# Performance work log

Measured on AMD Instinct MI355X. Metric: run time of the kernel, lower is better.

The kernel has to match this reference:

```python
import jax, jax.numpy as jnp
import numpy as np

RNN_HID = 64
INPUT_DIM = 35
SEQ_LEN = 48
BATCH = 4096


def setup_inputs() -> dict:
    key = jax.random.key(0)
    ks = jax.random.split(key, 16)
    x_t = jax.random.normal(ks[0], (BATCH, SEQ_LEN, INPUT_DIM), jnp.float32)
    masks = (jax.random.uniform(ks[1], (BATCH, SEQ_LEN, INPUT_DIM)) > 0.2).astype(jnp.float32)
    deltas = jax.random.uniform(ks[2], (BATCH, SEQ_LEN, INPUT_DIM), jnp.float32)
    evals = jax.random.normal(ks[3], (BATCH, SEQ_LEN, INPUT_DIM), jnp.float32)
    eval_masks = (jax.random.uniform(ks[4], (BATCH, SEQ_LEN, INPUT_DIM)) > 0.8).astype(jnp.float32)
    is_train = jnp.ones((BATCH,), jnp.float32)

    in_sz = INPUT_DIM * 2  # LSTMCell input = concat(x_c, m)
    s_lstm = 1.0 / np.sqrt(RNN_HID)
    # torch LSTMCell params: W_ih [4H, in], W_hh [4H, H], b_ih [4H], b_hh [4H]
    W_ih = jax.random.uniform(ks[5], (4 * RNN_HID, in_sz), jnp.float32, -s_lstm, s_lstm)
    W_hh = jax.random.uniform(ks[6], (4 * RNN_HID, RNN_HID), jnp.float32, -s_lstm, s_lstm)
    b_ih = jax.random.uniform(ks[7], (4 * RNN_HID,), jnp.float32, -s_lstm, s_lstm)
    b_hh = jax.random.uniform(ks[8], (4 * RNN_HID,), jnp.float32, -s_lstm, s_lstm)
    W_reg = jax.random.uniform(ks[9], (INPUT_DIM, RNN_HID), jnp.float32, -s_lstm, s_lstm)
    b_reg = jax.random.uniform(ks[10], (INPUT_DIM,), jnp.float32, -s_lstm, s_lstm)
    # TemporalDecay: W [RNN_HID, input_dim], b [RNN_HID]
    W_td = jax.random.uniform(ks[11], (RNN_HID, INPUT_DIM), jnp.float32, -s_lstm, s_lstm)
    b_td = jax.random.uniform(ks[12], (RNN_HID,), jnp.float32, -s_lstm, s_lstm)
    # out Linear(RNN_HID -> 1)
    W_out = jax.random.uniform(ks[13], (1, RNN_HID), jnp.float32, -s_lstm, s_lstm)
    b_out = jax.random.uniform(ks[14], (1,), jnp.float32, -s_lstm, s_lstm)
    return {
        'x_t': x_t, 'masks': masks, 'deltas': deltas, 'evals': evals,
        'eval_masks': eval_masks, 'is_train': is_train,
        'W_ih': W_ih, 'W_hh': W_hh, 'b_ih': b_ih, 'b_hh': b_hh,
        'W_reg': W_reg, 'b_reg': b_reg, 'W_td': W_td, 'b_td': b_td,
        'W_out': W_out, 'b_out': b_out,
    }


def _lstm_cell(inp, h, c, W_ih, W_hh, b_ih, b_hh):
    # gates ordered i, f, g, o as in torch.nn.LSTMCell
    gates = inp @ W_ih.T + h @ W_hh.T + b_ih + b_hh  # [B, 4H]
    i, f, g, o = jnp.split(gates, 4, axis=-1)
    i = jax.nn.sigmoid(i)
    f = jax.nn.sigmoid(f)
    g = jnp.tanh(g)
    o = jax.nn.sigmoid(o)
    c_new = f * c + i * g
    h_new = o * jnp.tanh(c_new)
    return h_new, c_new


def reference(x_t, masks, deltas, evals, eval_masks, is_train,
              W_ih, W_hh, b_ih, b_hh, W_reg, b_reg, W_td, b_td, W_out, b_out):
    B, T, D = x_t.shape
    h0 = jnp.zeros((B, RNN_HID), x_t.dtype)
    c0 = jnp.zeros((B, RNN_HID), x_t.dtype)

    def step(carry, xs):
        h, c, x_loss = carry
        x, m, d = xs  # each [B, D]
        x_hat = h @ W_reg.T + b_reg
        x_c = m * x + (1.0 - m) * x_hat
        x_loss = x_loss + jnp.sum(jnp.abs(x - x_hat) * m) / (jnp.sum(m) + 1e-5)
        inputs = jnp.concatenate([x_c, m], axis=1)  # [B, 2D]
        # temporal decay (computed as in original, result unused)
        gamma = jnp.exp(-jax.nn.relu(d @ W_td.T + b_td))
        h, c = _lstm_cell(inputs, h, c, W_ih, W_hh, b_ih, b_hh)
        return (h, c, x_loss), x_c

    xs = (jnp.swapaxes(x_t, 0, 1), jnp.swapaxes(masks, 0, 1), jnp.swapaxes(deltas, 0, 1))
    (h, c, x_loss), imp = jax.lax.scan(step, (h0, c0, jnp.float32(0.0)), xs)
    imputations = jnp.swapaxes(imp, 0, 1)  # [B, T, D]
    y_h = jax.nn.sigmoid(h @ W_out.T + b_out)
    loss = x_loss / T  # y_loss == 0
    return loss, y_h, imputations
```

## Files before the change

kernel.cpp:

```cpp
#include <hip/hip_runtime.h>
#include <stdint.h>

#define B_    4096
#define T_    48
#define D_    35
#define KROW  168
#define ROWEL (T_ * D_)
#define L2E   1.44269504f

typedef float f32x4 __attribute__((ext_vector_type(4)));
typedef short bf16x8 __attribute__((ext_vector_type(8)));

static __device__ __forceinline__ uint32_t fbits(float x){union{float f;uint32_t u;}v;v.f=x;return v.u;}
static __device__ __forceinline__ float bitsf(uint32_t u){union{uint32_t u;float f;}v;v.u=u;return v.f;}
static __device__ __forceinline__ float bf2f(unsigned short b){return bitsf(((uint32_t)b)<<16);}
static __device__ __forceinline__ unsigned short f2bf_rne(float x){
    uint32_t u=fbits(x); return (unsigned short)((u+0x7fffu+((u>>16)&1u))>>16);
}
static __device__ __forceinline__ float rcp_(float x){return __builtin_amdgcn_rcpf(x);}
static __device__ __forceinline__ float exp2_(float x){return __builtin_amdgcn_exp2f(x);}

#define MFMA __builtin_amdgcn_mfma_f32_16x16x32_bf16


__global__ __launch_bounds__(512, 1)
void brits_main(const float* __restrict__ x_t, const float* __restrict__ masks,
                const float* __restrict__ W_ih, const float* __restrict__ W_hh,
                const float* __restrict__ b_ih, const float* __restrict__ b_hh,
                const float* __restrict__ W_reg, const float* __restrict__ b_reg,
                const float* __restrict__ W_out, const float* __restrict__ b_out,
                float* __restrict__ ws, float* __restrict__ out)
{
    __shared__ __align__(16) unsigned short Abuf[2][16 * KROW];
    __shared__ __align__(16) unsigned short stash[16 * ROWEL];
    __shared__ unsigned long long mbits[16 * T_];
    __shared__ float lsum[T_ * 3 * 64];
    __shared__ float wout[65];

    const int tid    = threadIdx.x;
    const int lane   = tid & 63;
    const int w      = tid >> 6;
    const int g      = lane >> 4;
    const int cc     = lane & 15;
    const int batch0 = blockIdx.x * 16;
    const int u      = (w & 3) * 16 + cc;
    const int u2     = (w - 4) * 16 + cc;

    for (int i = tid; i < 16 * KROW; i += 512) ((uint32_t*)Abuf)[i] = 0;
    if (tid < 65) wout[tid] = (tid < 64) ? W_out[tid] : b_out[0];

    for (int i = tid; i < 16 * 210; i += 512) {
        const int r = i / 210;
        const int o = (i - r * 210) * 8;
        const float* xp = x_t   + (size_t)(batch0 + r) * ROWEL + o;
        const float* mp = masks + (size_t)(batch0 + r) * ROWEL + o;
        float xv[8], mv[8];
        *(float4*)&xv[0] = *(const float4*)xp; *(float4*)&xv[4] = *(const float4*)(xp + 4);
        *(float4*)&mv[0] = *(const float4*)mp; *(float4*)&mv[4] = *(const float4*)(mp + 4);
        unsigned short pk[8];
        #pragma unroll
        for (int k = 0; k < 8; ++k) pk[k] = f2bf_rne(mv[k] * xv[k]);
        *(uint4*)&stash[r * ROWEL + o] = *(const uint4*)pk;
    }
    for (int p = tid; p < 16 * T_; p += 512) {
        const int r = p / T_, t = p - r * T_;
        const float* mp = masks + (size_t)(batch0 + r) * ROWEL + t * D_;
        unsigned long long bits = 0;
        for (int d = 0; d < D_; ++d) bits |= (unsigned long long)(mp[d] != 0.f) << d;
        mbits[p] = bits;
    }

    bf16x8 Wf[4][5];
    float bIs = 0.f, bFs = 0.f, bGs = 0.f, bOs = 0.f;
    if (w < 4) {
        #pragma unroll
        for (int G = 0; G < 4; ++G) {
            const int n = G * 64 + u;
            #pragma unroll
            for (int kc = 0; kc < 5; ++kc) {
                bf16x8 v;
                #pragma unroll
                for (int i = 0; i < 8; ++i) {
                    const int k = kc * 32 + 8 * g + i;
                    float f = 0.f;
                    if (k < 70)                  f = W_ih[n * 70 + k];
                    else if (k >= 72 && k < 136) f = W_hh[n * 64 + (k - 72)];
                    v[i] = (short)f2bf_rne(f);
                }
                Wf[G][kc] = v;
            }
        }
        bIs = -(b_ih[u]       + b_hh[u])       * L2E;
        bFs = -(b_ih[64 + u]  + b_hh[64 + u])  * L2E;
        bGs = -(b_ih[128 + u] + b_hh[128 + u]) * 2.f * L2E;
        bOs = -(b_ih[192 + u] + b_hh[192 + u]) * L2E;
    }
    bf16x8 Wr0 = {0,0,0,0,0,0,0,0}, Wr1 = {0,0,0,0,0,0,0,0};
    float brg = 0.f;
    const bool pw = (w >= 4) && (w < 7);
    const bool pl = pw && (u2 < 35);
    if (pl) {
        #pragma unroll
        for (int i = 0; i < 8; ++i) {
            Wr0[i] = (short)f2bf_rne(W_reg[u2 * 64 + 8 * g + i]);
            Wr1[i] = (short)f2bf_rne(W_reg[u2 * 64 + 32 + 8 * g + i]);
        }
        brg = b_reg[u2];
    }
    __syncthreads();

    unsigned long long PM[4] = {0, 0, 0, 0};
    uint32_t xmr[4] = {0, 0, 0, 0};
    if (pl) {
        #pragma unroll
        for (int j = 0; j < 4; ++j) {
            const int row = 4 * g + j;
            unsigned long long pm = 0;
            for (int t = 0; t < T_; ++t)
                pm |= ((mbits[row * T_ + t] >> u2) & 1ull) << t;
            PM[j] = pm;
            xmr[j] = stash[row * ROWEL + u2];
            Abuf[0][row * KROW + 35 + u2] = (pm & 1ull) ? (unsigned short)0x3F80 : (unsigned short)0;
        }
    }
    __syncthreads();

    float c_[4] = {0.f, 0.f, 0.f, 0.f};

    for (int t = 0; t < T_; ++t) {
        unsigned short* A  = Abuf[t & 1];
        unsigned short* An = Abuf[(t + 1) & 1];

        f32x4 gI = {0,0,0,0}, gF = {0,0,0,0}, gG = {0,0,0,0}, gO = {0,0,0,0};

        if (w < 4) {
            bf16x8 a2 = *(const bf16x8*)&A[cc * KROW + 64  + 8 * g];
            bf16x8 a3 = *(const bf16x8*)&A[cc * KROW + 96  + 8 * g];
            bf16x8 a4 = *(const bf16x8*)&A[cc * KROW + 128 + 8 * g];
            gI = MFMA(a2, Wf[0][2], gI, 0,0,0);
            gF = MFMA(a2, Wf[1][2], gF, 0,0,0);
            gG = MFMA(a2, Wf[2][2], gG, 0,0,0);
            gO = MFMA(a2, Wf[3][2], gO, 0,0,0);
            gI = MFMA(a3, Wf[0][3], gI, 0,0,0);
            gF = MFMA(a3, Wf[1][3], gF, 0,0,0);
            gG = MFMA(a3, Wf[2][3], gG, 0,0,0);
            gO = MFMA(a3, Wf[3][3], gO, 0,0,0);
            gI = MFMA(a4, Wf[0][4], gI, 0,0,0);
            gF = MFMA(a4, Wf[1][4], gF, 0,0,0);
            gG = MFMA(a4, Wf[2][4], gG, 0,0,0);
            gO = MFMA(a4, Wf[3][4], gO, 0,0,0);
        } else if (pw) {
            bf16x8 ah0 = *(const bf16x8*)&A[cc * KROW + 72  + 8 * g];
            bf16x8 ah1 = *(const bf16x8*)&A[cc * KROW + 104 + 8 * g];
            f32x4 p0 = {0,0,0,0};
            p0 = MFMA(ah0, Wr0, p0, 0,0,0);
            p0 = MFMA(ah1, Wr1, p0, 0,0,0);
            float lnum = 0.f;
            if (u2 < 35) {
                #pragma unroll
                for (int j = 0; j < 4; ++j) {
                    const int row = 4 * g + j;
                    const float xh = p0[j] + brg;
                    const float xm = bf2f((unsigned short)xmr[j]);
                    const uint32_t mb = (uint32_t)(PM[j] >> t) & 1u;
                    lnum += mb ? fabsf(xm - xh) : 0.f;
                    const unsigned short xc16 = mb ? (unsigned short)xmr[j] : f2bf_rne(xh);
                    A[row * KROW + u2] = xc16;
                    An[row * KROW + 35 + u2] =
                        ((PM[j] >> (t + 1)) & 1ull) ? (unsigned short)0x3F80 : (unsigned short)0;
                    stash[row * ROWEL + t * D_ + u2] = xc16;
                }
            }
            lsum[(t * 3 + (w - 4)) * 64 + lane] = lnum;
        }
        __syncthreads();

        if (w < 4) {
            bf16x8 a0 = *(const bf16x8*)&A[cc * KROW + 0  + 8 * g];
            bf16x8 a1 = *(const bf16x8*)&A[cc * KROW + 32 + 8 * g];
            gI = MFMA(a0, Wf[0][0], gI, 0,0,0);
            gF = MFMA(a0, Wf[1][0], gF, 0,0,0);
            gG = MFMA(a0, Wf[2][0], gG, 0,0,0);
            gO = MFMA(a0, Wf[3][0], gO, 0,0,0);
            gI = MFMA(a1, Wf[0][1], gI, 0,0,0);
            gF = MFMA(a1, Wf[1][1], gF, 0,0,0);
            gG = MFMA(a1, Wf[2][1], gG, 0,0,0);
            gO = MFMA(a1, Wf[3][1], gO, 0,0,0);
            #pragma unroll
            for (int j = 0; j < 4; ++j) {
                const float iv = rcp_(1.f + exp2_(fmaf(gI[j], -L2E,       bIs)));
                const float fv = rcp_(1.f + exp2_(fmaf(gF[j], -L2E,       bFs)));
                const float gv = fmaf(2.f, rcp_(1.f + exp2_(fmaf(gG[j], -2.f * L2E, bGs))), -1.f);
                const float ov = rcp_(1.f + exp2_(fmaf(gO[j], -L2E,       bOs)));
                const float cn = fmaf(fv, c_[j], iv * gv);
                c_[j] = cn;
                const float th = fmaf(2.f, rcp_(1.f + exp2_(cn * (-2.f * L2E))), -1.f);
                An[(4 * g + j) * KROW + 72 + u] = (unsigned short)(fbits(ov * th) >> 16);
            }
        } else if (pl && t + 1 < T_) {
            #pragma unroll
            for (int j = 0; j < 4; ++j)
                xmr[j] = stash[(4 * g + j) * ROWEL + (t + 1) * D_ + u2];
        }
        __syncthreads();
    }

    if (tid < T_) {
        const int t = tid;
        float num = 0.f;
        for (int i = 0; i < 192; ++i) num += lsum[t * 192 + i];
        float den = 0.f;
        for (int r = 0; r < 16; ++r) den += (float)__popcll(mbits[r * T_ + t]);
        atomicAdd(&ws[t * 8 + (blockIdx.x & 7)], num);
        atomicAdd(&ws[(T_ + t) * 8 + (blockIdx.x & 7)], den);
    }

    if (w == 1) {
        float p = 0.f;
        #pragma unroll
        for (int k = 0; k < 16; ++k)
            p += bf2f(Abuf[0][cc * KROW + 72 + 16 * g + k]) * wout[16 * g + k];
        p += __shfl_xor(p, 16, 64);
        p += __shfl_xor(p, 32, 64);
        if (lane < 16) out[1 + batch0 + cc] = rcp_(1.f + exp2_(-(p + wout[64]) * L2E));
    }

    for (int i = tid; i < 16 * ROWEL; i += 512) {
        const int r = i / ROWEL;
        const int o = i - r * ROWEL;
        out[1 + B_ + (size_t)(batch0 + r) * ROWEL + o] = bf2f(stash[i]);
    }
}

__global__ void post_kernel(const float* __restrict__ ws, float* __restrict__ out)
{
    const int t = threadIdx.x;
    float v = 0.f;
    if (t < T_) {
        float num = 0.f, den = 0.f;
        #pragma unroll
        for (int s = 0; s < 8; ++s) {
            num += ws[t * 8 + s];
            den += ws[(T_ + t) * 8 + s];
        }
        v = num / (den + 1e-5f);
    }
    #pragma unroll
    for (int off = 1; off < 64; off <<= 1) v += __shfl_xor(v, off, 64);
    if (t == 0) out[0] = v * (1.0f / T_);
}

extern "C" void kernel_launch(void* const* d_in, const int* in_sizes, int n_in,
                              void* d_out, int out_size, void* d_ws, size_t ws_size,
                              hipStream_t stream) {
    const float* x_t   = (const float*)d_in[0];
    const float* masks = (const float*)d_in[1];
    const float* W_ih  = (const float*)d_in[6];
    const float* W_hh  = (const float*)d_in[7];
    const float* b_ih  = (const float*)d_in[8];
    const float* b_hh  = (const float*)d_in[9];
    const float* W_reg = (const float*)d_in[10];
    const float* b_reg = (const float*)d_in[11];
    const float* W_out = (const float*)d_in[14];
    const float* b_out = (const float*)d_in[15];
    float* out = (float*)d_out;
    float* ws  = (float*)d_ws;

    hipMemsetAsync(ws, 0, 2 * T_ * 8 * sizeof(float), stream);
    brits_main<<<B_ / 16, 512, 0, stream>>>(x_t, masks, W_ih, W_hh, b_ih, b_hh,
                                            W_reg, b_reg, W_out, b_out, ws, out);
    post_kernel<<<1, 64, 0, stream>>>(ws, out);
}
```

Baseline: 86.19 us.

## Shorten recurrent critical path by moving mask MFMAs and loss out of loop

The LSTM input row is reordered so h comes first. The mask-bit part of the gate matmul is now built in registers from the packed mask bits and issued before the barrier, together with the h@W_hh MFMAs. Only the x_c columns are left after the barrier, which shortens the serial per-timestep path. The per-step loss accumulation and bf16 rounding of x_c are deferred to the epilogue, using a second stash of x_hat and shared-memory atomics. This costs extra LDS for the x_hat stash and adds atomic contention in the epilogue. x_hat is also now truncated to bf16 instead of rounded to nearest even.

```diff
diff --git a/kernel.cpp b/kernel.cpp
--- a/kernel.cpp
+++ b/kernel.cpp
@@ -4,22 +4,23 @@
 #define B_    4096
 #define T_    48
 #define D_    35
-#define KROW  168
-#define ROWEL (T_ * D_)
+#define KR    136
+#define MBS   49
+#define ROWEL 1680
 #define L2E   1.44269504f
 
 typedef float f32x4 __attribute__((ext_vector_type(4)));
 typedef short bf16x8 __attribute__((ext_vector_type(8)));
+union U4 { uint32_t u[4]; bf16x8 v; };
 
 static __device__ __forceinline__ uint32_t fbits(float x){union{float f;uint32_t u;}v;v.f=x;return v.u;}
 static __device__ __forceinline__ float bitsf(uint32_t u){union{uint32_t u;float f;}v;v.u=u;return v.f;}
-static __device__ __forceinline__ float bf2f(unsigned short b){return bitsf(((uint32_t)b)<<16);}
+static __device__ __forceinline__ float bf2f(uint32_t b){return bitsf(b<<16);}
 static __device__ __forceinline__ unsigned short f2bf_rne(float x){
     uint32_t u=fbits(x); return (unsigned short)((u+0x7fffu+((u>>16)&1u))>>16);
 }
 static __device__ __forceinline__ float rcp_(float x){return __builtin_amdgcn_rcpf(x);}
 static __device__ __forceinline__ float exp2_(float x){return __builtin_amdgcn_exp2f(x);}
-
 #define MFMA __builtin_amdgcn_mfma_f32_16x16x32_bf16
 
 
@@ -31,11 +32,12 @@
                 const float* __restrict__ W_out, const float* __restrict__ b_out,
                 float* __restrict__ ws, float* __restrict__ out)
 {
-    __shared__ __align__(16) unsigned short Abuf[2][16 * KROW];
-    __shared__ __align__(16) unsigned short stash[16 * ROWEL];
-    __shared__ unsigned long long mbits[16 * T_];
-    __shared__ float lsum[T_ * 3 * 64];
-    __shared__ float wout[65];
+    __shared__ __align__(16) unsigned short stash [16 * ROWEL];
+    __shared__ __align__(16) unsigned short stash2[16 * ROWEL];
+    __shared__ __align__(16) unsigned short Abuf[2][16 * KR];
+    __shared__ unsigned long long mbitsP[16 * MBS];
+    __shared__ float lossb[T_ * 8];
+    __shared__ float wout[68];
 
     const int tid    = threadIdx.x;
     const int lane   = tid & 63;
@@ -46,8 +48,9 @@
     const int u      = (w & 3) * 16 + cc;
     const int u2     = (w - 4) * 16 + cc;
 
-    for (int i = tid; i < 16 * KROW; i += 512) ((uint32_t*)Abuf)[i] = 0;
-    if (tid < 65) wout[tid] = (tid < 64) ? W_out[tid] : b_out[0];
+    for (int i = tid; i < 16 * KR; i += 512) ((uint32_t*)Abuf)[i] = 0;
+    if (tid < 65)  wout[tid]  = (tid < 64) ? W_out[tid] : b_out[0];
+    if (tid < 384) lossb[tid] = 0.f;
 
     for (int i = tid; i < 16 * 210; i += 512) {
         const int r = i / 210;
@@ -67,24 +70,27 @@
         const float* mp = masks + (size_t)(batch0 + r) * ROWEL + t * D_;
         unsigned long long bits = 0;
         for (int d = 0; d < D_; ++d) bits |= (unsigned long long)(mp[d] != 0.f) << d;
-        mbits[p] = bits;
-    }
-
-    bf16x8 Wf[4][5];
+        mbitsP[r * MBS + t] = bits;
+    }
+
+    bf16x8 Wf[4][6];
     float bIs = 0.f, bFs = 0.f, bGs = 0.f, bOs = 0.f;
     if (w < 4) {
         #pragma unroll
         for (int G = 0; G < 4; ++G) {
             const int n = G * 64 + u;
             #pragma unroll
-            for (int kc = 0; kc < 5; ++kc) {
+            for (int kc = 0; kc < 6; ++kc) {
                 bf16x8 v;
                 #pragma unroll
                 for (int i = 0; i < 8; ++i) {
-                    const int k = kc * 32 + 8 * g + i;
                     float f = 0.f;
-                    if (k < 70)                  f = W_ih[n * 70 + k];
-                    else if (k >= 72 && k < 136) f = W_hh[n * 64 + (k - 72)];
+                    if (kc == 0)      f = W_hh[n * 64 + 8 * g + i];
+                    else if (kc == 1) f = W_hh[n * 64 + 32 + 8 * g + i];
+                    else if (kc == 2) f = W_ih[n * 70 + 8 * g + i];
+                    else if (kc == 3) { if (g == 0 && i < 3) f = W_ih[n * 70 + 32 + i]; }
+                    else if (kc == 4) f = W_ih[n * 70 + 35 + 8 * g + i];
+                    else              { if (g == 0 && i < 3) f = W_ih[n * 70 + 67 + i]; }
                     v[i] = (short)f2bf_rne(f);
                 }
                 Wf[G][kc] = v;
@@ -95,10 +101,10 @@
         bGs = -(b_ih[128 + u] + b_hh[128 + u]) * 2.f * L2E;
         bOs = -(b_ih[192 + u] + b_hh[192 + u]) * L2E;
     }
+    const bool pw = (w >= 4) && (w < 7);
+    const bool pl = pw && (u2 < 35);
     bf16x8 Wr0 = {0,0,0,0,0,0,0,0}, Wr1 = {0,0,0,0,0,0,0,0};
     float brg = 0.f;
-    const bool pw = (w >= 4) && (w < 7);
-    const bool pl = pw && (u2 < 35);
     if (pl) {
         #pragma unroll
         for (int i = 0; i < 8; ++i) {
@@ -117,13 +123,11 @@
             const int row = 4 * g + j;
             unsigned long long pm = 0;
             for (int t = 0; t < T_; ++t)
-                pm |= ((mbits[row * T_ + t] >> u2) & 1ull) << t;
+                pm |= ((mbitsP[row * MBS + t] >> u2) & 1ull) << t;
             PM[j] = pm;
             xmr[j] = stash[row * ROWEL + u2];
-            Abuf[0][row * KROW + 35 + u2] = (pm & 1ull) ? (unsigned short)0x3F80 : (unsigned short)0;
-        }
-    }
-    __syncthreads();
+        }
+    }
 
     float c_[4] = {0.f, 0.f, 0.f, 0.f};
 
@@ -134,9 +138,64 @@
         f32x4 gI = {0,0,0,0}, gF = {0,0,0,0}, gG = {0,0,0,0}, gO = {0,0,0,0};
 
         if (w < 4) {
-            bf16x8 a2 = *(const bf16x8*)&A[cc * KROW + 64  + 8 * g];
-            bf16x8 a3 = *(const bf16x8*)&A[cc * KROW + 96  + 8 * g];
-            bf16x8 a4 = *(const bf16x8*)&A[cc * KROW + 128 + 8 * g];
+            const bf16x8 ah0 = *(const bf16x8*)&A[cc * KR + 8 * g];
+            const bf16x8 ah1 = *(const bf16x8*)&A[cc * KR + 32 + 8 * g];
+            const unsigned long long mb = mbitsP[cc * MBS + t];
+            U4 c2f;
+            #pragma unroll
+            for (int ii = 0; ii < 4; ++ii) {
+                const uint32_t b2 = (uint32_t)(mb >> (8 * g + 2 * ii)) & 3u;
+                c2f.u[ii] = ((b2 & 1u) ? 0x3F80u : 0u) | ((b2 & 2u) ? 0x3F800000u : 0u);
+            }
+            U4 c5f;
+            if (g == 0) {
+                const uint32_t b32 = (uint32_t)(mb >> 32) & 1u;
+                const uint32_t b33 = (uint32_t)(mb >> 33) & 1u;
+                const uint32_t b34 = (uint32_t)(mb >> 34) & 1u;
+                c5f.u[0] = (b32 ? 0x3F80u : 0u) | (b33 ? 0x3F800000u : 0u);
+                c5f.u[1] = (b34 ? 0x3F80u : 0u);
+                c5f.u[2] = 0; c5f.u[3] = 0;
+            } else { c5f.u[0] = c5f.u[1] = c5f.u[2] = c5f.u[3] = 0; }
+
+            gI = MFMA(c2f.v, Wf[0][4], gI, 0,0,0);
+            gF = MFMA(c2f.v, Wf[1][4], gF, 0,0,0);
+            gG = MFMA(c2f.v, Wf[2][4], gG, 0,0,0);
+            gO = MFMA(c2f.v, Wf[3][4], gO, 0,0,0);
+            gI = MFMA(c5f.v, Wf[0][5], gI, 0,0,0);
+            gF = MFMA(c5f.v, Wf[1][5], gF, 0,0,0);
+            gG = MFMA(c5f.v, Wf[2][5], gG, 0,0,0);
+            gO = MFMA(c5f.v, Wf[3][5], gO, 0,0,0);
+            gI = MFMA(ah0, Wf[0][0], gI, 0,0,0);
+            gF = MFMA(ah0, Wf[1][0], gF, 0,0,0);
+            gG = MFMA(ah0, Wf[2][0], gG, 0,0,0);
+            gO = MFMA(ah0, Wf[3][0], gO, 0,0,0);
+            gI = MFMA(ah1, Wf[0][1], gI, 0,0,0);
+            gF = MFMA(ah1, Wf[1][1], gF, 0,0,0);
+            gG = MFMA(ah1, Wf[2][1], gG, 0,0,0);
+            gO = MFMA(ah1, Wf[3][1], gO, 0,0,0);
+        } else if (pw) {
+            const bf16x8 ah0 = *(const bf16x8*)&A[cc * KR + 8 * g];
+            const bf16x8 ah1 = *(const bf16x8*)&A[cc * KR + 32 + 8 * g];
+            f32x4 p0 = {0,0,0,0};
+            p0 = MFMA(ah0, Wr0, p0, 0,0,0);
+            p0 = MFMA(ah1, Wr1, p0, 0,0,0);
+            if (pl) {
+                #pragma unroll
+                for (int j = 0; j < 4; ++j) {
+                    const int row = 4 * g + j;
+                    const float xh = p0[j] + brg;
+                    const uint32_t xhb = fbits(xh) >> 16;
+                    stash2[row * ROWEL + t * D_ + u2] = (unsigned short)xhb;
+                    const uint32_t bit = (uint32_t)(PM[j] >> t) & 1u;
+                    A[row * KR + 64 + u2] = (unsigned short)(bit ? xmr[j] : xhb);
+                }
+            }
+        }
+        __syncthreads();
+
+        if (w < 4) {
+            const bf16x8 a2 = *(const bf16x8*)&A[cc * KR + 64 + 8 * g];
+            const bf16x8 a3 = *(const bf16x8*)&A[cc * KR + 96 + 8 * g];
             gI = MFMA(a2, Wf[0][2], gI, 0,0,0);
             gF = MFMA(a2, Wf[1][2], gF, 0,0,0);
             gG = MFMA(a2, Wf[2][2], gG, 0,0,0);
@@ -145,47 +204,6 @@
             gF = MFMA(a3, Wf[1][3], gF, 0,0,0);
             gG = MFMA(a3, Wf[2][3], gG, 0,0,0);
             gO = MFMA(a3, Wf[3][3], gO, 0,0,0);
-            gI = MFMA(a4, Wf[0][4], gI, 0,0,0);
-            gF = MFMA(a4, Wf[1][4], gF, 0,0,0);
-            gG = MFMA(a4, Wf[2][4], gG, 0,0,0);
-            gO = MFMA(a4, Wf[3][4], gO, 0,0,0);
-        } else if (pw) {
-            bf16x8 ah0 = *(const bf16x8*)&A[cc * KROW + 72  + 8 * g];
-            bf16x8 ah1 = *(const bf16x8*)&A[cc * KROW + 104 + 8 * g];
-            f32x4 p0 = {0,0,0,0};
-            p0 = MFMA(ah0, Wr0, p0, 0,0,0);
-            p0 = MFMA(ah1, Wr1, p0, 0,0,0);
-            float lnum = 0.f;
-            if (u2 < 35) {
-                #pragma unroll
-                for (int j = 0; j < 4; ++j) {
-                    const int row = 4 * g + j;
-                    const float xh = p0[j] + brg;
-                    const float xm = bf2f((unsigned short)xmr[j]);
-                    const uint32_t mb = (uint32_t)(PM[j] >> t) & 1u;
-                    lnum += mb ? fabsf(xm - xh) : 0.f;
-                    const unsigned short xc16 = mb ? (unsigned short)xmr[j] : f2bf_rne(xh);
-                    A[row * KROW + u2] = xc16;
-                    An[row * KROW + 35 + u2] =
-                        ((PM[j] >> (t + 1)) & 1ull) ? (unsigned short)0x3F80 : (unsigned short)0;
-                    stash[row * ROWEL + t * D_ + u2] = xc16;
-                }
-            }
-            lsum[(t * 3 + (w - 4)) * 64 + lane] = lnum;
-        }
-        __syncthreads();
-
-        if (w < 4) {
-            bf16x8 a0 = *(const bf16x8*)&A[cc * KROW + 0  + 8 * g];
-            bf16x8 a1 = *(const bf16x8*)&A[cc * KROW + 32 + 8 * g];
-            gI = MFMA(a0, Wf[0][0], gI, 0,0,0);
-            gF = MFMA(a0, Wf[1][0], gF, 0,0,0);
-            gG = MFMA(a0, Wf[2][0], gG, 0,0,0);
-            gO = MFMA(a0, Wf[3][0], gO, 0,0,0);
-            gI = MFMA(a1, Wf[0][1], gI, 0,0,0);
-            gF = MFMA(a1, Wf[1][1], gF, 0,0,0);
-            gG = MFMA(a1, Wf[2][1], gG, 0,0,0);
-            gO = MFMA(a1, Wf[3][1], gO, 0,0,0);
             #pragma unroll
             for (int j = 0; j < 4; ++j) {
                 const float iv = rcp_(1.f + exp2_(fmaf(gI[j], -L2E,       bIs)));
@@ -195,7 +213,7 @@
                 const float cn = fmaf(fv, c_[j], iv * gv);
                 c_[j] = cn;
                 const float th = fmaf(2.f, rcp_(1.f + exp2_(cn * (-2.f * L2E))), -1.f);
-                An[(4 * g + j) * KROW + 72 + u] = (unsigned short)(fbits(ov * th) >> 16);
+                An[(4 * g + j) * KR + u] = (unsigned short)(fbits(ov * th) >> 16);
             }
         } else if (pl && t + 1 < T_) {
             #pragma unroll
@@ -205,21 +223,11 @@
         __syncthreads();
     }
 
-    if (tid < T_) {
-        const int t = tid;
-        float num = 0.f;
-        for (int i = 0; i < 192; ++i) num += lsum[t * 192 + i];
-        float den = 0.f;
-        for (int r = 0; r < 16; ++r) den += (float)__popcll(mbits[r * T_ + t]);
-        atomicAdd(&ws[t * 8 + (blockIdx.x & 7)], num);
-        atomicAdd(&ws[(T_ + t) * 8 + (blockIdx.x & 7)], den);
-    }
-
-    if (w == 1) {
+    if (w == 0) {
         float p = 0.f;
         #pragma unroll
         for (int k = 0; k < 16; ++k)
-            p += bf2f(Abuf[0][cc * KROW + 72 + 16 * g + k]) * wout[16 * g + k];
+            p += bf2f(Abuf[0][cc * KR + 16 * g + k]) * wout[16 * g + k];
         p += __shfl_xor(p, 16, 64);
         p += __shfl_xor(p, 32, 64);
         if (lane < 16) out[1 + batch0 + cc] = rcp_(1.f + exp2_(-(p + wout[64]) * L2E));
@@ -228,7 +236,22 @@
     for (int i = tid; i < 16 * ROWEL; i += 512) {
         const int r = i / ROWEL;
         const int o = i - r * ROWEL;
-        out[1 + B_ + (size_t)(batch0 + r) * ROWEL + o] = bf2f(stash[i]);
+        const int t = o / D_, d = o - D_ * t;
+        const uint32_t mx = stash[i];
+        const uint32_t xh = stash2[i];
+        const uint32_t bit = (uint32_t)(mbitsP[r * MBS + t] >> d) & 1u;
+        out[1 + B_ + (size_t)(batch0 + r) * ROWEL + o] = bf2f(bit ? mx : xh);
+        if (bit) atomicAdd(&lossb[t * 8 + (tid & 7)], fabsf(bf2f(mx) - bf2f(xh)));
+    }
+    __syncthreads();
+    if (tid < T_) {
+        float num = 0.f;
+        #pragma unroll
+        for (int s = 0; s < 8; ++s) num += lossb[tid * 8 + s];
+        float den = 0.f;
+        for (int r = 0; r < 16; ++r) den += (float)__popcll(mbitsP[r * MBS + tid]);
+        atomicAdd(&ws[tid * 8 + (blockIdx.x & 7)], num);
+        atomicAdd(&ws[(T_ + tid) * 8 + (blockIdx.x & 7)], den);
     }
 }
 
```

After: 106.0 us. 1.23x slower.

## Stream imputations to global per step, split MFMA accumulators, use lightweight barriers

Applied to the files above, without the earlier changes.

Each imputed value is now written straight to global memory inside the recurrence loop rather than staged in LDS and copied out after the loop, so the output stores overlap with the serial time-step chain. The gate accumulators are split into two independent chains summed at the end, which shortens MFMA dependency latency. __syncthreads is replaced by a custom barrier that waits only on LDS counters (lgkmcnt) and not on outstanding global stores. The global stores are scattered (stride D per step, one element per lane), which may give poorly coalesced writes, and the custom barrier depends on stash no longer being written inside the loop.

```diff
diff --git a/kernel.cpp b/kernel.cpp
--- a/kernel.cpp
+++ b/kernel.cpp
@@ -13,14 +13,19 @@
 
 static __device__ __forceinline__ uint32_t fbits(float x){union{float f;uint32_t u;}v;v.f=x;return v.u;}
 static __device__ __forceinline__ float bitsf(uint32_t u){union{uint32_t u;float f;}v;v.u=u;return v.f;}
-static __device__ __forceinline__ float bf2f(unsigned short b){return bitsf(((uint32_t)b)<<16);}
+static __device__ __forceinline__ float bf2f(uint32_t b){return bitsf(b<<16);}
 static __device__ __forceinline__ unsigned short f2bf_rne(float x){
     uint32_t u=fbits(x); return (unsigned short)((u+0x7fffu+((u>>16)&1u))>>16);
 }
 static __device__ __forceinline__ float rcp_(float x){return __builtin_amdgcn_rcpf(x);}
 static __device__ __forceinline__ float exp2_(float x){return __builtin_amdgcn_exp2f(x);}
-
 #define MFMA __builtin_amdgcn_mfma_f32_16x16x32_bf16
+
+static __device__ __forceinline__ void step_barrier() {
+    asm volatile("s_waitcnt lgkmcnt(0)" ::: "memory");
+    __builtin_amdgcn_s_barrier();
+    __builtin_amdgcn_sched_barrier(0);
+}
 
 
 __global__ __launch_bounds__(512, 1)
@@ -111,6 +116,7 @@
 
     unsigned long long PM[4] = {0, 0, 0, 0};
     uint32_t xmr[4] = {0, 0, 0, 0};
+    float* orow[4];
     if (pl) {
         #pragma unroll
         for (int j = 0; j < 4; ++j) {
@@ -121,6 +127,7 @@
             PM[j] = pm;
             xmr[j] = stash[row * ROWEL + u2];
             Abuf[0][row * KROW + 35 + u2] = (pm & 1ull) ? (unsigned short)0x3F80 : (unsigned short)0;
+            orow[j] = out + 1 + B_ + (size_t)(batch0 + row) * ROWEL + u2;
         }
     }
     __syncthreads();
@@ -131,24 +138,25 @@
         unsigned short* A  = Abuf[t & 1];
         unsigned short* An = Abuf[(t + 1) & 1];
 
-        f32x4 gI = {0,0,0,0}, gF = {0,0,0,0}, gG = {0,0,0,0}, gO = {0,0,0,0};
+        f32x4 gIa = {0,0,0,0}, gFa = {0,0,0,0}, gGa = {0,0,0,0}, gOa = {0,0,0,0};
+        f32x4 gIb = {0,0,0,0}, gFb = {0,0,0,0}, gGb = {0,0,0,0}, gOb = {0,0,0,0};
 
         if (w < 4) {
             bf16x8 a2 = *(const bf16x8*)&A[cc * KROW + 64  + 8 * g];
             bf16x8 a3 = *(const bf16x8*)&A[cc * KROW + 96  + 8 * g];
             bf16x8 a4 = *(const bf16x8*)&A[cc * KROW + 128 + 8 * g];
-            gI = MFMA(a2, Wf[0][2], gI, 0,0,0);
-            gF = MFMA(a2, Wf[1][2], gF, 0,0,0);
-            gG = MFMA(a2, Wf[2][2], gG, 0,0,0);
-            gO = MFMA(a2, Wf[3][2], gO, 0,0,0);
-            gI = MFMA(a3, Wf[0][3], gI, 0,0,0);
-            gF = MFMA(a3, Wf[1][3], gF, 0,0,0);
-            gG = MFMA(a3, Wf[2][3], gG, 0,0,0);
-            gO = MFMA(a3, Wf[3][3], gO, 0,0,0);
-            gI = MFMA(a4, Wf[0][4], gI, 0,0,0);
-            gF = MFMA(a4, Wf[1][4], gF, 0,0,0);
-            gG = MFMA(a4, Wf[2][4], gG, 0,0,0);
-            gO = MFMA(a4, Wf[3][4], gO, 0,0,0);
+            gIa = MFMA(a2, Wf[0][2], gIa, 0,0,0);
+            gFa = MFMA(a2, Wf[1][2], gFa, 0,0,0);
+            gGa = MFMA(a2, Wf[2][2], gGa, 0,0,0);
+            gOa = MFMA(a2, Wf[3][2], gOa, 0,0,0);
+            gIb = MFMA(a3, Wf[0][3], gIb, 0,0,0);
+            gFb = MFMA(a3, Wf[1][3], gFb, 0,0,0);
+            gGb = MFMA(a3, Wf[2][3], gGb, 0,0,0);
+            gOb = MFMA(a3, Wf[3][3], gOb, 0,0,0);
+            gIa = MFMA(a4, Wf[0][4], gIa, 0,0,0);
+            gFa = MFMA(a4, Wf[1][4], gFa, 0,0,0);
+            gGa = MFMA(a4, Wf[2][4], gGa, 0,0,0);
+            gOa = MFMA(a4, Wf[3][4], gOa, 0,0,0);
         } else if (pw) {
             bf16x8 ah0 = *(const bf16x8*)&A[cc * KROW + 72  + 8 * g];
             bf16x8 ah1 = *(const bf16x8*)&A[cc * KROW + 104 + 8 * g];
@@ -156,36 +164,40 @@
             p0 = MFMA(ah0, Wr0, p0, 0,0,0);
             p0 = MFMA(ah1, Wr1, p0, 0,0,0);
             float lnum = 0.f;
-            if (u2 < 35) {
+            if (pl) {
                 #pragma unroll
                 for (int j = 0; j < 4; ++j) {
                     const int row = 4 * g + j;
                     const float xh = p0[j] + brg;
-                    const float xm = bf2f((unsigned short)xmr[j]);
+                    const float xm = bf2f(xmr[j]);
                     const uint32_t mb = (uint32_t)(PM[j] >> t) & 1u;
                     lnum += mb ? fabsf(xm - xh) : 0.f;
                     const unsigned short xc16 = mb ? (unsigned short)xmr[j] : f2bf_rne(xh);
                     A[row * KROW + u2] = xc16;
                     An[row * KROW + 35 + u2] =
                         ((PM[j] >> (t + 1)) & 1ull) ? (unsigned short)0x3F80 : (unsigned short)0;
-                    stash[row * ROWEL + t * D_ + u2] = xc16;
+                    orow[j][t * D_] = bf2f((uint32_t)xc16);
                 }
             }
             lsum[(t * 3 + (w - 4)) * 64 + lane] = lnum;
         }
-        __syncthreads();
+        step_barrier();
 
         if (w < 4) {
             bf16x8 a0 = *(const bf16x8*)&A[cc * KROW + 0  + 8 * g];
             bf16x8 a1 = *(const bf16x8*)&A[cc * KROW + 32 + 8 * g];
-            gI = MFMA(a0, Wf[0][0], gI, 0,0,0);
-            gF = MFMA(a0, Wf[1][0], gF, 0,0,0);
-            gG = MFMA(a0, Wf[2][0], gG, 0,0,0);
-            gO = MFMA(a0, Wf[3][0], gO, 0,0,0);
-            gI = MFMA(a1, Wf[0][1], gI, 0,0,0);
-            gF = MFMA(a1, Wf[1][1], gF, 0,0,0);
-            gG = MFMA(a1, Wf[2][1], gG, 0,0,0);
-            gO = MFMA(a1, Wf[3][1], gO, 0,0,0);
+            gIa = MFMA(a0, Wf[0][0], gIa, 0,0,0);
+            gFa = MFMA(a0, Wf[1][0], gFa, 0,0,0);
+            gGa = MFMA(a0, Wf[2][0], gGa, 0,0,0);
+            gOa = MFMA(a0, Wf[3][0], gOa, 0,0,0);
+            gIb = MFMA(a1, Wf[0][1], gIb, 0,0,0);
+            gFb = MFMA(a1, Wf[1][1], gFb, 0,0,0);
+            gGb = MFMA(a1, Wf[2][1], gGb, 0,0,0);
+            gOb = MFMA(a1, Wf[3][1], gOb, 0,0,0);
+            const f32x4 gI = gIa + gIb;
+            const f32x4 gF = gFa + gFb;
+            const f32x4 gG = gGa + gGb;
+            const f32x4 gO = gOa + gOb;
             #pragma unroll
             for (int j = 0; j < 4; ++j) {
                 const float iv = rcp_(1.f + exp2_(fmaf(gI[j], -L2E,       bIs)));
@@ -202,8 +214,10 @@
             for (int j = 0; j < 4; ++j)
                 xmr[j] = stash[(4 * g + j) * ROWEL + (t + 1) * D_ + u2];
         }
-        __syncthreads();
-    }
+        step_barrier();
+    }
+
+    __syncthreads();
 
     if (tid < T_) {
         const int t = tid;
@@ -223,12 +237,6 @@
         p += __shfl_xor(p, 16, 64);
         p += __shfl_xor(p, 32, 64);
         if (lane < 16) out[1 + batch0 + cc] = rcp_(1.f + exp2_(-(p + wout[64]) * L2E));
-    }
-
-    for (int i = tid; i < 16 * ROWEL; i += 512) {
-        const int r = i / ROWEL;
-        const int o = i - r * ROWEL;
-        out[1 + B_ + (size_t)(batch0 + r) * ROWEL + o] = bf2f(stash[i]);
     }
 }
 
```

Measured after the change: 86.66 us. No clear change (+0.6%).
